# Optimization experiments

Measured on AMD Instinct MI355X. Metric: run time of the kernel, lower is better.

The kernel has to match this reference:

```python
import jax, jax.numpy as jnp
import numpy as np

NUM_VARS = 64
LAG = 16
H1 = 64
H2 = 1024
NUM_OUT = 1
BATCH = 16384


def setup_inputs() -> dict:
    key = jax.random.key(0)
    ks = jax.random.split(key, 8)

    def xavier(k, shape, fan_in, fan_out):
        std = float(np.sqrt(2.0 / (fan_in + fan_out)))
        return jax.random.normal(k, shape, dtype=jnp.float32) * std

    inputs = jax.random.normal(ks[0], (BATCH, NUM_VARS * LAG), dtype=jnp.float32)
    # Per-variable sub-network weights, batched over the variable axis.
    W1 = xavier(ks[1], (NUM_VARS, LAG, H1), LAG, H1)
    b1 = jnp.full((NUM_VARS, H1), 0.1, dtype=jnp.float32)
    W2 = xavier(ks[2], (NUM_VARS, H1, H1), H1, H1)
    b2 = jnp.full((NUM_VARS, H1), 0.1, dtype=jnp.float32)
    imp = (jnp.ones((NUM_VARS,), dtype=jnp.float32) / NUM_VARS
           + 1e-5 * jax.random.normal(ks[3], (NUM_VARS,), dtype=jnp.float32))
    W3 = xavier(ks[4], (NUM_VARS * H1, H2), NUM_VARS * H1, H2)
    b3 = jnp.full((H2,), 0.1, dtype=jnp.float32)
    W4 = xavier(ks[5], (H2, NUM_OUT), H2, NUM_OUT)
    b4 = jnp.full((NUM_OUT,), 0.1, dtype=jnp.float32)
    return {"inputs": inputs, "W1": W1, "b1": b1, "W2": W2, "b2": b2,
            "imp": imp, "W3": W3, "b3": b3, "W4": W4, "b4": b4}


def reference(inputs, W1, b1, W2, b2, imp, W3, b3, W4, b4):
    B = inputs.shape[0]
    # [B, V*lag] -> [B, V, lag]; slicing inputs[:, lag*i:lag*(i+1)] == x[:, i, :]
    x = inputs.reshape(B, NUM_VARS, LAG)
    # dp = 0.0 -> dropout is identity
    h = jax.nn.relu(jnp.einsum('bvl,vlh->bvh', x, W1) + b1[None])      # [B, V, H1]
    h = jax.nn.relu(jnp.einsum('bvh,vhk->bvk', h, W2) + b2[None])      # [B, V, H1]
    agg = (h * imp[None, :, None]).reshape(B, NUM_VARS * H1)            # weighted concat
    pred = jax.nn.relu(agg @ W3 + b3) @ W4 + b4                        # [B, NUM_OUT]
    return pred
```

## Files before the change

### kernel.cpp

```cpp
#include <hip/hip_runtime.h>
#include <hip/hip_bf16.h>
#include <stdint.h>

#define B_ROWS 16384
#define NVARS 64
#define LAG 16
#define H1 64
#define H2 1024
#define KDIM (NVARS * H1)

typedef __attribute__((ext_vector_type(8))) short short8;
typedef __attribute__((ext_vector_type(4))) short short4v;
typedef __attribute__((ext_vector_type(4))) float f32x4;

typedef __attribute__((address_space(3))) uint8_t lds_u8;
typedef const __attribute__((address_space(1))) uint8_t glob_u8;

__device__ __forceinline__ void gload_lds16(const void* g, void* l) {
    __builtin_amdgcn_global_load_lds((glob_u8*)g, (lds_u8*)l, 16, 0, 0);
}

__device__ __forceinline__ short f2bf_s(float x) {
    __hip_bfloat16 h = __float2bfloat16(x);
    return *(short*)&h;
}
__device__ __forceinline__ float bf_s2f(short s) {
    __hip_bfloat16 h = *(__hip_bfloat16*)&s;
    return __bfloat162float(h);
}

__global__ __launch_bounds__(256) void convert_w3t_kernel(
    const float* __restrict__ w3, __hip_bfloat16* __restrict__ w3t) {
    __shared__ float tile[64][65];
    const int bx = blockIdx.x;
    const int k0 = (bx >> 4) * 64;
    const int n0 = (bx & 15) * 64;
    const int t = threadIdx.x;
    const int c = t & 63, r0 = t >> 6;
#pragma unroll
    for (int i = 0; i < 16; i++) {
        int r = r0 + i * 4;
        tile[r][c] = w3[(size_t)(k0 + r) * H2 + n0 + c];
    }
    __syncthreads();
#pragma unroll
    for (int i = 0; i < 16; i++) {
        int nr = r0 + i * 4;
        w3t[(size_t)(n0 + nr) * KDIM + k0 + c] = __float2bfloat16(tile[c][nr]);
    }
}

__global__ __launch_bounds__(256) void prep_w12_kernel(
    const float* __restrict__ W1, const float* __restrict__ W2,
    short* __restrict__ w1bh, short* __restrict__ w1bl,
    short* __restrict__ w2bh, short* __restrict__ w2bl) {
    const int v = blockIdx.x, t = threadIdx.x;
    for (int idx = t; idx < 64 * 32; idx += 256) {
        int col = idx >> 5, k = idx & 31;
        float wv = W1[((size_t)v * LAG + (k & 15)) * H1 + col];
        short hi = f2bf_s(wv);
        w1bh[((size_t)v * 64 + col) * 40 + k] = hi;
        w1bl[((size_t)v * 64 + col) * 40 + k] = (k < 16) ? f2bf_s(wv - bf_s2f(hi)) : (short)0;
    }
    for (int idx = t; idx < 64 * 64; idx += 256) {
        int col = idx >> 6, k = idx & 63;
        float wv = W2[((size_t)v * H1 + k) * H1 + col];
        short hi = f2bf_s(wv);
        w2bh[((size_t)v * 64 + col) * 72 + k] = hi;
        w2bl[((size_t)v * 64 + col) * 72 + k] = f2bf_s(wv - bf_s2f(hi));
    }
}

__global__ __launch_bounds__(256) void out_init_kernel(
    const float* __restrict__ b4, float* __restrict__ out) {
    out[blockIdx.x * 256 + threadIdx.x] = b4[0];
}

__global__ __launch_bounds__(256) void subnets_mfma_kernel(
    const float* __restrict__ inputs, const float* __restrict__ b1g,
    const float* __restrict__ b2g, const float* __restrict__ impg,
    const short* __restrict__ w1bh_g, const short* __restrict__ w1bl_g,
    const short* __restrict__ w2bh_g, const short* __restrict__ w2bl_g,
    __hip_bfloat16* __restrict__ agg) {
    const int v = blockIdx.x >> 7;
    const int b0 = (blockIdx.x & 127) * 128;
    const int t = threadIdx.x;
    const int lane = t & 63, wv = t >> 6;
    const int l15 = lane & 15, g = lane >> 4;

    __shared__ __align__(16) char smem[53248];
    short* xsS   = (short*)smem;
    short* w1bhS = (short*)(smem + 10240);
    short* w1blS = (short*)(smem + 15360);
    short* Hs    = (short*)smem;
    short* w2bhS = (short*)(smem + 34816);
    short* w2blS = (short*)(smem + 44032);

    for (int c = t; c < 320; c += 256) {
        gload_lds16(w1bh_g + (size_t)v * 2560 + c * 8, (char*)w1bhS + c * 16);
        gload_lds16(w1bl_g + (size_t)v * 2560 + c * 8, (char*)w1blS + c * 16);
    }
    for (int c = t; c < 576; c += 256) {
        gload_lds16(w2bh_g + (size_t)v * 4608 + c * 8, (char*)w2bhS + c * 16);
        gload_lds16(w2bl_g + (size_t)v * 4608 + c * 8, (char*)w2blS + c * 16);
    }
#pragma unroll
    for (int i = 0; i < 2; i++) {
        int idx = t + i * 256;
        int row = idx >> 2, seg = idx & 3;
        float4 x4 = *(const float4*)(inputs + (size_t)(b0 + row) * (NVARS * LAG) + v * LAG + seg * 4);
        const float* xp = (const float*)&x4;
        short4v hv, lv;
#pragma unroll
        for (int j = 0; j < 4; j++) {
            short hi = f2bf_s(xp[j]);
            hv[j] = hi;
            lv[j] = f2bf_s(xp[j] - bf_s2f(hi));
        }
        *(short4v*)&xsS[row * 40 + seg * 4] = hv;
        *(short4v*)&xsS[row * 40 + 16 + seg * 4] = lv;
    }
    __syncthreads();

    short8 a1[2], b1hF[4], b1lF[4];
#pragma unroll
    for (int mt = 0; mt < 2; mt++)
        a1[mt] = *(const short8*)&xsS[(wv * 32 + mt * 16 + l15) * 40 + g * 8];
#pragma unroll
    for (int nt = 0; nt < 4; nt++) {
        b1hF[nt] = *(const short8*)&w1bhS[(nt * 16 + l15) * 40 + g * 8];
        b1lF[nt] = *(const short8*)&w1blS[(nt * 16 + l15) * 40 + g * 8];
    }
    f32x4 acc1[2][4];
#pragma unroll
    for (int mt = 0; mt < 2; mt++)
#pragma unroll
        for (int nt = 0; nt < 4; nt++) {
            acc1[mt][nt] = (f32x4){0.f, 0.f, 0.f, 0.f};
            acc1[mt][nt] = __builtin_amdgcn_mfma_f32_16x16x32_bf16(a1[mt], b1hF[nt], acc1[mt][nt], 0, 0, 0);
            acc1[mt][nt] = __builtin_amdgcn_mfma_f32_16x16x32_bf16(a1[mt], b1lF[nt], acc1[mt][nt], 0, 0, 0);
        }
    __syncthreads();

#pragma unroll
    for (int mt = 0; mt < 2; mt++)
#pragma unroll
        for (int nt = 0; nt < 4; nt++) {
            int col = nt * 16 + l15;
            float bias = b1g[v * H1 + col];
#pragma unroll
            for (int r = 0; r < 4; r++) {
                float h = fmaxf(acc1[mt][nt][r] + bias, 0.f);
                short hi = f2bf_s(h);
                short lo = f2bf_s(h - bf_s2f(hi));
                int row = wv * 32 + mt * 16 + g * 4 + r;
                Hs[row * 136 + col] = hi;
                Hs[row * 136 + 64 + col] = lo;
            }
        }
    __syncthreads();

    short8 a2[2][4], b2hF[4][2], b2lF[4][2];
#pragma unroll
    for (int mt = 0; mt < 2; mt++)
#pragma unroll
        for (int c = 0; c < 4; c++)
            a2[mt][c] = *(const short8*)&Hs[(wv * 32 + mt * 16 + l15) * 136 + c * 32 + g * 8];
#pragma unroll
    for (int nt = 0; nt < 4; nt++)
#pragma unroll
        for (int kc = 0; kc < 2; kc++) {
            b2hF[nt][kc] = *(const short8*)&w2bhS[(nt * 16 + l15) * 72 + kc * 32 + g * 8];
            b2lF[nt][kc] = *(const short8*)&w2blS[(nt * 16 + l15) * 72 + kc * 32 + g * 8];
        }
    f32x4 acc2[2][4];
#pragma unroll
    for (int mt = 0; mt < 2; mt++)
#pragma unroll
        for (int nt = 0; nt < 4; nt++) {
            f32x4 a = (f32x4){0.f, 0.f, 0.f, 0.f};
            a = __builtin_amdgcn_mfma_f32_16x16x32_bf16(a2[mt][0], b2hF[nt][0], a, 0, 0, 0);
            a = __builtin_amdgcn_mfma_f32_16x16x32_bf16(a2[mt][1], b2hF[nt][1], a, 0, 0, 0);
            a = __builtin_amdgcn_mfma_f32_16x16x32_bf16(a2[mt][2], b2hF[nt][0], a, 0, 0, 0);
            a = __builtin_amdgcn_mfma_f32_16x16x32_bf16(a2[mt][3], b2hF[nt][1], a, 0, 0, 0);
            a = __builtin_amdgcn_mfma_f32_16x16x32_bf16(a2[mt][0], b2lF[nt][0], a, 0, 0, 0);
            a = __builtin_amdgcn_mfma_f32_16x16x32_bf16(a2[mt][1], b2lF[nt][1], a, 0, 0, 0);
            acc2[mt][nt] = a;
        }

    const float impv = impg[v];
#pragma unroll
    for (int mt = 0; mt < 2; mt++)
#pragma unroll
        for (int nt = 0; nt < 4; nt++) {
            int col = nt * 16 + l15;
            float bias = b2g[v * H1 + col];
#pragma unroll
            for (int r = 0; r < 4; r++) {
                float o = fmaxf(acc2[mt][nt][r] + bias, 0.f) * impv;
                int row = b0 + wv * 32 + mt * 16 + g * 4 + r;
                agg[(size_t)row * KDIM + v * H1 + col] = __float2bfloat16(o);
            }
        }
}

#define NT 128

__global__ __launch_bounds__(512, 2) void gemm3_kernel(
    const __hip_bfloat16* __restrict__ agg,
    const __hip_bfloat16* __restrict__ w3t,
    const float* __restrict__ b3, const float* __restrict__ W4,
    float* __restrict__ out) {
    const int bid = ((blockIdx.x & 7) << 5) + (blockIdx.x >> 3);
    const int brow = (bid >> 2) * 256;
    const int bcol = (bid & 3) * 256;
    const int t = threadIdx.x;
    const int lane = t & 63;
    const int wid = t >> 6;
    const int wm = wid >> 2, wn = wid & 3;
    const int l15 = lane & 15, g = lane >> 4;

    __shared__ __align__(16) char smem[131072];

    const int c0 = t, c1 = t + 512;
    const int r0 = c0 >> 2, r1 = c1 >> 2;
    const int col0 = ((c0 & 3) * 8) ^ ((r0 & 8) ? 16 : 0);
    const int col1 = ((c1 & 3) * 8) ^ ((r1 & 8) ? 16 : 0);
    const __hip_bfloat16* aS0 = agg + (size_t)(brow + r0) * KDIM + col0;
    const __hip_bfloat16* aS1 = agg + (size_t)(brow + r1) * KDIM + col1;
    const __hip_bfloat16* bS0 = w3t + (size_t)(bcol + r0) * KDIM + col0;
    const __hip_bfloat16* bS1 = w3t + (size_t)(bcol + r1) * KDIM + col1;

#define STAGE_A(p, kt) do { \
        gload_lds16(aS0 + (kt) * 32, smem + (p) * 32768 + c0 * 16); \
        gload_lds16(aS1 + (kt) * 32, smem + (p) * 32768 + c1 * 16); } while (0)
#define STAGE_B(p, kt) do { \
        gload_lds16(bS0 + (kt) * 32, smem + (p) * 32768 + 16384 + c0 * 16); \
        gload_lds16(bS1 + (kt) * 32, smem + (p) * 32768 + 16384 + c1 * 16); } while (0)

    const int coff = (g * 16) ^ ((l15 & 8) ? 32 : 0);
    const int aBase = (wm * 128 + l15) * 64 + coff;
    const int bBase = 16384 + (wn * 64 + l15) * 64 + coff;

#define LDA(i, p) fa[i] = *(const short8*)(smem + (p) * 32768 + aBase + (i) * 1024)
#define LDB(i, p) fb[i] = *(const short8*)(smem + (p) * 32768 + bBase + (i) * 1024)

    short8 fa[8], fb[4];
    f32x4 acc[8][4];
#pragma unroll
    for (int m = 0; m < 8; m++)
#pragma unroll
        for (int n = 0; n < 4; n++) acc[m][n] = (f32x4){0.f, 0.f, 0.f, 0.f};

    STAGE_A(0, 0); STAGE_B(0, 0);
    STAGE_A(1, 1); STAGE_B(1, 1);
    STAGE_A(2, 2); STAGE_B(2, 2);
    asm volatile("s_waitcnt vmcnt(8)" ::: "memory");
    __builtin_amdgcn_s_barrier();

#define PH_A(p, DOSTAGE, kt3) do { \
        LDA(0, p); LDA(1, p); LDA(2, p); LDA(3, p); \
        LDB(0, p); LDB(1, p); LDB(2, p); LDB(3, p); \
        if (DOSTAGE) STAGE_A((kt3) & 3, kt3); \
        __builtin_amdgcn_s_barrier(); \
        asm volatile("s_waitcnt lgkmcnt(0)" ::: "memory"); \
        __builtin_amdgcn_sched_barrier(0); \
        __builtin_amdgcn_s_setprio(1); \
        _Pragma("unroll") \
        for (int mm = 0; mm < 4; mm++) \
            _Pragma("unroll") \
            for (int nn = 0; nn < 4; nn++) \
                acc[mm][nn] = __builtin_amdgcn_mfma_f32_16x16x32_bf16( \
                    fa[mm], fb[nn], acc[mm][nn], 0, 0, 0); \
        __builtin_amdgcn_s_setprio(0); \
        __builtin_amdgcn_s_barrier(); } while (0)

#define PH_B(p, DOSTAGE, kt3, VMSTR) do { \
        LDA(4, p); LDA(5, p); LDA(6, p); LDA(7, p); \
        if (DOSTAGE) STAGE_B((kt3) & 3, kt3); \
        asm volatile(VMSTR ::: "memory"); \
        __builtin_amdgcn_s_barrier(); \
        asm volatile("s_waitcnt lgkmcnt(0)" ::: "memory"); \
        __builtin_amdgcn_sched_barrier(0); \
        __builtin_amdgcn_s_setprio(1); \
        _Pragma("unroll") \
        for (int mm = 0; mm < 4; mm++) \
            _Pragma("unroll") \
            for (int nn = 0; nn < 4; nn++) \
                acc[4 + mm][nn] = __builtin_amdgcn_mfma_f32_16x16x32_bf16( \
                    fa[4 + mm], fb[nn], acc[4 + mm][nn], 0, 0, 0); \
        __builtin_amdgcn_s_setprio(0); \
        __builtin_amdgcn_s_barrier(); } while (0)

#pragma unroll 4
    for (int tt = 0; tt < NT - 4; ++tt) {
        const int p = tt & 3;
        PH_A(p, 1, tt + 3);
        PH_B(p, 1, tt + 3, "s_waitcnt vmcnt(8)");
    }
    PH_A(0, 1, 127); PH_B(0, 1, 127, "s_waitcnt vmcnt(8)");
    PH_A(1, 0, 0);   PH_B(1, 0, 0, "s_waitcnt vmcnt(4)");
    PH_A(2, 0, 0);   PH_B(2, 0, 0, "s_waitcnt vmcnt(0)");
    PH_A(3, 0, 0);   PH_B(3, 0, 0, "s_waitcnt vmcnt(0)");

    float bias[4], w4v[4];
#pragma unroll
    for (int n = 0; n < 4; n++) {
        int col = bcol + wn * 64 + n * 16 + l15;
        bias[n] = b3[col];
        w4v[n] = W4[col];
    }
#pragma unroll
    for (int m = 0; m < 8; m++) {
        float pr0 = 0.f, pr1 = 0.f, pr2 = 0.f, pr3 = 0.f;
#pragma unroll
        for (int n = 0; n < 4; n++) {
            pr0 += fmaxf(acc[m][n][0] + bias[n], 0.f) * w4v[n];
            pr1 += fmaxf(acc[m][n][1] + bias[n], 0.f) * w4v[n];
            pr2 += fmaxf(acc[m][n][2] + bias[n], 0.f) * w4v[n];
            pr3 += fmaxf(acc[m][n][3] + bias[n], 0.f) * w4v[n];
        }
#pragma unroll
        for (int mask = 1; mask < 16; mask <<= 1) {
            pr0 += __shfl_xor(pr0, mask, 64);
            pr1 += __shfl_xor(pr1, mask, 64);
            pr2 += __shfl_xor(pr2, mask, 64);
            pr3 += __shfl_xor(pr3, mask, 64);
        }
        if (l15 == 0) {
            int row = brow + wm * 128 + m * 16 + g * 4;
            atomicAdd(&out[row + 0], pr0);
            atomicAdd(&out[row + 1], pr1);
            atomicAdd(&out[row + 2], pr2);
            atomicAdd(&out[row + 3], pr3);
        }
    }
}

extern "C" void kernel_launch(void* const* d_in, const int* in_sizes, int n_in,
                              void* d_out, int out_size, void* d_ws, size_t ws_size,
                              hipStream_t stream) {
    const float* inputs = (const float*)d_in[0];
    const float* W1 = (const float*)d_in[1];
    const float* b1 = (const float*)d_in[2];
    const float* W2 = (const float*)d_in[3];
    const float* b2 = (const float*)d_in[4];
    const float* imp = (const float*)d_in[5];
    const float* W3 = (const float*)d_in[6];
    const float* b3 = (const float*)d_in[7];
    const float* W4 = (const float*)d_in[8];
    const float* b4 = (const float*)d_in[9];
    float* out = (float*)d_out;

    char* ws = (char*)d_ws;
    const size_t agg_bytes  = (size_t)B_ROWS * KDIM * 2;
    const size_t w3t_bytes  = (size_t)H2 * KDIM * 2;
    const size_t w1b_bytes  = (size_t)NVARS * 64 * 40 * 2;
    const size_t w2b_bytes  = (size_t)NVARS * 64 * 72 * 2;

    __hip_bfloat16* agg = (__hip_bfloat16*)ws;
    __hip_bfloat16* w3t = (__hip_bfloat16*)(ws + agg_bytes);
    short* w1bh = (short*)(ws + agg_bytes + w3t_bytes);
    short* w1bl = (short*)(ws + agg_bytes + w3t_bytes + w1b_bytes);
    short* w2bh = (short*)(ws + agg_bytes + w3t_bytes + 2 * w1b_bytes);
    short* w2bl = (short*)(ws + agg_bytes + w3t_bytes + 2 * w1b_bytes + w2b_bytes);

    hipLaunchKernelGGL(convert_w3t_kernel, dim3(1024), dim3(256), 0, stream, W3, w3t);
    hipLaunchKernelGGL(prep_w12_kernel, dim3(NVARS), dim3(256), 0, stream,
                       W1, W2, w1bh, w1bl, w2bh, w2bl);
    hipLaunchKernelGGL(out_init_kernel, dim3(B_ROWS / 256), dim3(256), 0, stream, b4, out);
    hipLaunchKernelGGL(subnets_mfma_kernel, dim3(NVARS * (B_ROWS / 128)), dim3(256), 0, stream,
                       inputs, b1, b2, imp, w1bh, w1bl, w2bh, w2bl, agg);
    hipLaunchKernelGGL(gemm3_kernel, dim3((B_ROWS / 256) * (H2 / 256)), dim3(512), 0, stream,
                       agg, w3t, b3, W4, out);
}
```

Before: 181.4 us.

## Fuse preprocessing kernels into one launch and cut GEMM pipeline barriers

Merges the W3 transpose/convert, the output bias init and the subnet kernel into a single launch, dispatched by block-index ranges. W1/W2 are now split into hi/lo bf16 directly into LDS inside each subnet block, which removes the separate prep kernel and its workspace round trip at the cost of redundant per-block conversion. In the GEMM main loop, the per-phase barriers and explicit lgkmcnt waits are replaced by a single vmcnt wait plus barrier at the end of each iteration. This relies on the 4-deep buffer ring to keep LDS staging writes away from buffers still being read.

```diff
diff --git a/kernel.cpp b/kernel.cpp
--- a/kernel.cpp
+++ b/kernel.cpp
@@ -29,66 +29,46 @@
     return __bfloat162float(h);
 }
 
-__global__ __launch_bounds__(256) void convert_w3t_kernel(
-    const float* __restrict__ w3, __hip_bfloat16* __restrict__ w3t) {
-    __shared__ float tile[64][65];
-    const int bx = blockIdx.x;
-    const int k0 = (bx >> 4) * 64;
-    const int n0 = (bx & 15) * 64;
+__global__ __launch_bounds__(256) void fused_pre_kernel(
+    const float* __restrict__ inputs, const float* __restrict__ W1,
+    const float* __restrict__ b1g, const float* __restrict__ W2,
+    const float* __restrict__ b2g, const float* __restrict__ impg,
+    const float* __restrict__ w3, const float* __restrict__ b4,
+    __hip_bfloat16* __restrict__ w3t, __hip_bfloat16* __restrict__ agg,
+    float* __restrict__ out) {
+    __shared__ __align__(16) char smem[53248];
+    const int bid = blockIdx.x;
     const int t = threadIdx.x;
-    const int c = t & 63, r0 = t >> 6;
-#pragma unroll
-    for (int i = 0; i < 16; i++) {
-        int r = r0 + i * 4;
-        tile[r][c] = w3[(size_t)(k0 + r) * H2 + n0 + c];
-    }
-    __syncthreads();
-#pragma unroll
-    for (int i = 0; i < 16; i++) {
-        int nr = r0 + i * 4;
-        w3t[(size_t)(n0 + nr) * KDIM + k0 + c] = __float2bfloat16(tile[c][nr]);
-    }
-}
-
-__global__ __launch_bounds__(256) void prep_w12_kernel(
-    const float* __restrict__ W1, const float* __restrict__ W2,
-    short* __restrict__ w1bh, short* __restrict__ w1bl,
-    short* __restrict__ w2bh, short* __restrict__ w2bl) {
-    const int v = blockIdx.x, t = threadIdx.x;
-    for (int idx = t; idx < 64 * 32; idx += 256) {
-        int col = idx >> 5, k = idx & 31;
-        float wv = W1[((size_t)v * LAG + (k & 15)) * H1 + col];
-        short hi = f2bf_s(wv);
-        w1bh[((size_t)v * 64 + col) * 40 + k] = hi;
-        w1bl[((size_t)v * 64 + col) * 40 + k] = (k < 16) ? f2bf_s(wv - bf_s2f(hi)) : (short)0;
-    }
-    for (int idx = t; idx < 64 * 64; idx += 256) {
-        int col = idx >> 6, k = idx & 63;
-        float wv = W2[((size_t)v * H1 + k) * H1 + col];
-        short hi = f2bf_s(wv);
-        w2bh[((size_t)v * 64 + col) * 72 + k] = hi;
-        w2bl[((size_t)v * 64 + col) * 72 + k] = f2bf_s(wv - bf_s2f(hi));
-    }
-}
-
-__global__ __launch_bounds__(256) void out_init_kernel(
-    const float* __restrict__ b4, float* __restrict__ out) {
-    out[blockIdx.x * 256 + threadIdx.x] = b4[0];
-}
-
-__global__ __launch_bounds__(256) void subnets_mfma_kernel(
-    const float* __restrict__ inputs, const float* __restrict__ b1g,
-    const float* __restrict__ b2g, const float* __restrict__ impg,
-    const short* __restrict__ w1bh_g, const short* __restrict__ w1bl_g,
-    const short* __restrict__ w2bh_g, const short* __restrict__ w2bl_g,
-    __hip_bfloat16* __restrict__ agg) {
-    const int v = blockIdx.x >> 7;
-    const int b0 = (blockIdx.x & 127) * 128;
-    const int t = threadIdx.x;
+
+    if (bid < 1024) {
+        float (*tile)[65] = (float (*)[65])smem;
+        const int k0 = (bid >> 4) * 64;
+        const int n0 = (bid & 15) * 64;
+        const int c = t & 63, r0 = t >> 6;
+#pragma unroll
+        for (int i = 0; i < 16; i++) {
+            int r = r0 + i * 4;
+            tile[r][c] = w3[(size_t)(k0 + r) * H2 + n0 + c];
+        }
+        __syncthreads();
+#pragma unroll
+        for (int i = 0; i < 16; i++) {
+            int nr = r0 + i * 4;
+            w3t[(size_t)(n0 + nr) * KDIM + k0 + c] = __float2bfloat16(tile[c][nr]);
+        }
+        return;
+    }
+    if (bid < 1088) {
+        out[(bid - 1024) * 256 + t] = b4[0];
+        return;
+    }
+
+    const int sbid = bid - 1088;
+    const int v = sbid >> 7;
+    const int b0 = (sbid & 127) * 128;
     const int lane = t & 63, wv = t >> 6;
     const int l15 = lane & 15, g = lane >> 4;
 
-    __shared__ __align__(16) char smem[53248];
     short* xsS   = (short*)smem;
     short* w1bhS = (short*)(smem + 10240);
     short* w1blS = (short*)(smem + 15360);
@@ -96,13 +76,21 @@
     short* w2bhS = (short*)(smem + 34816);
     short* w2blS = (short*)(smem + 44032);
 
-    for (int c = t; c < 320; c += 256) {
-        gload_lds16(w1bh_g + (size_t)v * 2560 + c * 8, (char*)w1bhS + c * 16);
-        gload_lds16(w1bl_g + (size_t)v * 2560 + c * 8, (char*)w1blS + c * 16);
-    }
-    for (int c = t; c < 576; c += 256) {
-        gload_lds16(w2bh_g + (size_t)v * 4608 + c * 8, (char*)w2bhS + c * 16);
-        gload_lds16(w2bl_g + (size_t)v * 4608 + c * 8, (char*)w2blS + c * 16);
+    for (int idx = t; idx < LAG * H1; idx += 256) {
+        int l = idx >> 6, col = idx & 63;
+        float w = W1[(size_t)v * (LAG * H1) + idx];
+        short hi = f2bf_s(w), lo = f2bf_s(w - bf_s2f(hi));
+        w1bhS[col * 40 + l] = hi;
+        w1bhS[col * 40 + 16 + l] = hi;
+        w1blS[col * 40 + l] = lo;
+        w1blS[col * 40 + 16 + l] = 0;
+    }
+    for (int idx = t; idx < H1 * H1; idx += 256) {
+        int k = idx >> 6, col = idx & 63;
+        float w = W2[(size_t)v * (H1 * H1) + idx];
+        short hi = f2bf_s(w), lo = f2bf_s(w - bf_s2f(hi));
+        w2bhS[col * 72 + k] = hi;
+        w2blS[col * 72 + k] = lo;
     }
 #pragma unroll
     for (int i = 0; i < 2; i++) {
@@ -257,14 +245,12 @@
     STAGE_A(2, 2); STAGE_B(2, 2);
     asm volatile("s_waitcnt vmcnt(8)" ::: "memory");
     __builtin_amdgcn_s_barrier();
+    __builtin_amdgcn_sched_barrier(0);
 
 #define PH_A(p, DOSTAGE, kt3) do { \
         LDA(0, p); LDA(1, p); LDA(2, p); LDA(3, p); \
         LDB(0, p); LDB(1, p); LDB(2, p); LDB(3, p); \
         if (DOSTAGE) STAGE_A((kt3) & 3, kt3); \
-        __builtin_amdgcn_s_barrier(); \
-        asm volatile("s_waitcnt lgkmcnt(0)" ::: "memory"); \
-        __builtin_amdgcn_sched_barrier(0); \
         __builtin_amdgcn_s_setprio(1); \
         _Pragma("unroll") \
         for (int mm = 0; mm < 4; mm++) \
@@ -272,16 +258,11 @@
             for (int nn = 0; nn < 4; nn++) \
                 acc[mm][nn] = __builtin_amdgcn_mfma_f32_16x16x32_bf16( \
                     fa[mm], fb[nn], acc[mm][nn], 0, 0, 0); \
-        __builtin_amdgcn_s_setprio(0); \
-        __builtin_amdgcn_s_barrier(); } while (0)
+        __builtin_amdgcn_s_setprio(0); } while (0)
 
 #define PH_B(p, DOSTAGE, kt3, VMSTR) do { \
         LDA(4, p); LDA(5, p); LDA(6, p); LDA(7, p); \
         if (DOSTAGE) STAGE_B((kt3) & 3, kt3); \
-        asm volatile(VMSTR ::: "memory"); \
-        __builtin_amdgcn_s_barrier(); \
-        asm volatile("s_waitcnt lgkmcnt(0)" ::: "memory"); \
-        __builtin_amdgcn_sched_barrier(0); \
         __builtin_amdgcn_s_setprio(1); \
         _Pragma("unroll") \
         for (int mm = 0; mm < 4; mm++) \
@@ -290,7 +271,9 @@
                 acc[4 + mm][nn] = __builtin_amdgcn_mfma_f32_16x16x32_bf16( \
                     fa[4 + mm], fb[nn], acc[4 + mm][nn], 0, 0, 0); \
         __builtin_amdgcn_s_setprio(0); \
-        __builtin_amdgcn_s_barrier(); } while (0)
+        asm volatile(VMSTR ::: "memory"); \
+        __builtin_amdgcn_s_barrier(); \
+        __builtin_amdgcn_sched_barrier(0); } while (0)
 
 #pragma unroll 4
     for (int tt = 0; tt < NT - 4; ++tt) {
@@ -353,24 +336,12 @@
     float* out = (float*)d_out;
 
     char* ws = (char*)d_ws;
-    const size_t agg_bytes  = (size_t)B_ROWS * KDIM * 2;
-    const size_t w3t_bytes  = (size_t)H2 * KDIM * 2;
-    const size_t w1b_bytes  = (size_t)NVARS * 64 * 40 * 2;
-    const size_t w2b_bytes  = (size_t)NVARS * 64 * 72 * 2;
-
+    const size_t agg_bytes = (size_t)B_ROWS * KDIM * 2;
     __hip_bfloat16* agg = (__hip_bfloat16*)ws;
     __hip_bfloat16* w3t = (__hip_bfloat16*)(ws + agg_bytes);
-    short* w1bh = (short*)(ws + agg_bytes + w3t_bytes);
-    short* w1bl = (short*)(ws + agg_bytes + w3t_bytes + w1b_bytes);
-    short* w2bh = (short*)(ws + agg_bytes + w3t_bytes + 2 * w1b_bytes);
-    short* w2bl = (short*)(ws + agg_bytes + w3t_bytes + 2 * w1b_bytes + w2b_bytes);
-
-    hipLaunchKernelGGL(convert_w3t_kernel, dim3(1024), dim3(256), 0, stream, W3, w3t);
-    hipLaunchKernelGGL(prep_w12_kernel, dim3(NVARS), dim3(256), 0, stream,
-                       W1, W2, w1bh, w1bl, w2bh, w2bl);
-    hipLaunchKernelGGL(out_init_kernel, dim3(B_ROWS / 256), dim3(256), 0, stream, b4, out);
-    hipLaunchKernelGGL(subnets_mfma_kernel, dim3(NVARS * (B_ROWS / 128)), dim3(256), 0, stream,
-                       inputs, b1, b2, imp, w1bh, w1bl, w2bh, w2bl, agg);
+
+    hipLaunchKernelGGL(fused_pre_kernel, dim3(1088 + NVARS * (B_ROWS / 128)), dim3(256), 0, stream,
+                       inputs, W1, b1, W2, b2, imp, W3, b4, w3t, agg, out);
     hipLaunchKernelGGL(gemm3_kernel, dim3((B_ROWS / 256) * (H2 / 256)), dim3(512), 0, stream,
                        agg, w3t, b3, W4, out);
 }
```

Result: no change. 184.4 us (+1.6%).

## Cut gemm3 pipeline barriers to one per k-step and merge prep kernels

Applied to the files above, without the earlier changes.

The main W3 GEMM loop previously used four workgroup barriers per k-step, plus explicit lgkmcnt waits before each MFMA block. It now has a single barrier and vmcnt wait at the end of each k-step, relying on the 4-deep LDS ring to keep staging writes from racing with reads. Separately, the W3 transpose/convert, W1/W2 split-bf16 prep and output bias init kernels are fused into one launch that dispatches on block index, saving two launches. The looser sync lets waves drift apart more. Correctness depends on the ring-buffer reuse distance being large enough.

```diff
diff --git a/kernel.cpp b/kernel.cpp
--- a/kernel.cpp
+++ b/kernel.cpp
@@ -29,32 +29,39 @@
     return __bfloat162float(h);
 }
 
-__global__ __launch_bounds__(256) void convert_w3t_kernel(
-    const float* __restrict__ w3, __hip_bfloat16* __restrict__ w3t) {
-    __shared__ float tile[64][65];
-    const int bx = blockIdx.x;
-    const int k0 = (bx >> 4) * 64;
-    const int n0 = (bx & 15) * 64;
-    const int t = threadIdx.x;
-    const int c = t & 63, r0 = t >> 6;
-#pragma unroll
-    for (int i = 0; i < 16; i++) {
-        int r = r0 + i * 4;
-        tile[r][c] = w3[(size_t)(k0 + r) * H2 + n0 + c];
-    }
-    __syncthreads();
-#pragma unroll
-    for (int i = 0; i < 16; i++) {
-        int nr = r0 + i * 4;
-        w3t[(size_t)(n0 + nr) * KDIM + k0 + c] = __float2bfloat16(tile[c][nr]);
-    }
-}
-
-__global__ __launch_bounds__(256) void prep_w12_kernel(
+__global__ __launch_bounds__(256) void misc_pre_kernel(
+    const float* __restrict__ w3, const float* __restrict__ b4,
     const float* __restrict__ W1, const float* __restrict__ W2,
+    __hip_bfloat16* __restrict__ w3t, float* __restrict__ out,
     short* __restrict__ w1bh, short* __restrict__ w1bl,
     short* __restrict__ w2bh, short* __restrict__ w2bl) {
-    const int v = blockIdx.x, t = threadIdx.x;
+    __shared__ float tile[64][65];
+    const int bid = blockIdx.x;
+    const int t = threadIdx.x;
+
+    if (bid < 1024) {
+        const int k0 = (bid >> 4) * 64;
+        const int n0 = (bid & 15) * 64;
+        const int c = t & 63, r0 = t >> 6;
+#pragma unroll
+        for (int i = 0; i < 16; i++) {
+            int r = r0 + i * 4;
+            tile[r][c] = w3[(size_t)(k0 + r) * H2 + n0 + c];
+        }
+        __syncthreads();
+#pragma unroll
+        for (int i = 0; i < 16; i++) {
+            int nr = r0 + i * 4;
+            w3t[(size_t)(n0 + nr) * KDIM + k0 + c] = __float2bfloat16(tile[c][nr]);
+        }
+        return;
+    }
+    if (bid < 1088) {
+        out[(bid - 1024) * 256 + t] = b4[0];
+        return;
+    }
+
+    const int v = bid - 1088;
     for (int idx = t; idx < 64 * 32; idx += 256) {
         int col = idx >> 5, k = idx & 31;
         float wv = W1[((size_t)v * LAG + (k & 15)) * H1 + col];
@@ -69,11 +76,6 @@
         w2bh[((size_t)v * 64 + col) * 72 + k] = hi;
         w2bl[((size_t)v * 64 + col) * 72 + k] = f2bf_s(wv - bf_s2f(hi));
     }
-}
-
-__global__ __launch_bounds__(256) void out_init_kernel(
-    const float* __restrict__ b4, float* __restrict__ out) {
-    out[blockIdx.x * 256 + threadIdx.x] = b4[0];
 }
 
 __global__ __launch_bounds__(256) void subnets_mfma_kernel(
@@ -257,14 +259,12 @@
     STAGE_A(2, 2); STAGE_B(2, 2);
     asm volatile("s_waitcnt vmcnt(8)" ::: "memory");
     __builtin_amdgcn_s_barrier();
+    __builtin_amdgcn_sched_barrier(0);
 
 #define PH_A(p, DOSTAGE, kt3) do { \
         LDA(0, p); LDA(1, p); LDA(2, p); LDA(3, p); \
         LDB(0, p); LDB(1, p); LDB(2, p); LDB(3, p); \
         if (DOSTAGE) STAGE_A((kt3) & 3, kt3); \
-        __builtin_amdgcn_s_barrier(); \
-        asm volatile("s_waitcnt lgkmcnt(0)" ::: "memory"); \
-        __builtin_amdgcn_sched_barrier(0); \
         __builtin_amdgcn_s_setprio(1); \
         _Pragma("unroll") \
         for (int mm = 0; mm < 4; mm++) \
@@ -272,16 +272,11 @@
             for (int nn = 0; nn < 4; nn++) \
                 acc[mm][nn] = __builtin_amdgcn_mfma_f32_16x16x32_bf16( \
                     fa[mm], fb[nn], acc[mm][nn], 0, 0, 0); \
-        __builtin_amdgcn_s_setprio(0); \
-        __builtin_amdgcn_s_barrier(); } while (0)
+        __builtin_amdgcn_s_setprio(0); } while (0)
 
 #define PH_B(p, DOSTAGE, kt3, VMSTR) do { \
         LDA(4, p); LDA(5, p); LDA(6, p); LDA(7, p); \
         if (DOSTAGE) STAGE_B((kt3) & 3, kt3); \
-        asm volatile(VMSTR ::: "memory"); \
-        __builtin_amdgcn_s_barrier(); \
-        asm volatile("s_waitcnt lgkmcnt(0)" ::: "memory"); \
-        __builtin_amdgcn_sched_barrier(0); \
         __builtin_amdgcn_s_setprio(1); \
         _Pragma("unroll") \
         for (int mm = 0; mm < 4; mm++) \
@@ -290,7 +285,9 @@
                 acc[4 + mm][nn] = __builtin_amdgcn_mfma_f32_16x16x32_bf16( \
                     fa[4 + mm], fb[nn], acc[4 + mm][nn], 0, 0, 0); \
         __builtin_amdgcn_s_setprio(0); \
-        __builtin_amdgcn_s_barrier(); } while (0)
+        asm volatile(VMSTR ::: "memory"); \
+        __builtin_amdgcn_s_barrier(); \
+        __builtin_amdgcn_sched_barrier(0); } while (0)
 
 #pragma unroll 4
     for (int tt = 0; tt < NT - 4; ++tt) {
@@ -353,10 +350,10 @@
     float* out = (float*)d_out;
 
     char* ws = (char*)d_ws;
-    const size_t agg_bytes  = (size_t)B_ROWS * KDIM * 2;
-    const size_t w3t_bytes  = (size_t)H2 * KDIM * 2;
-    const size_t w1b_bytes  = (size_t)NVARS * 64 * 40 * 2;
-    const size_t w2b_bytes  = (size_t)NVARS * 64 * 72 * 2;
+    const size_t agg_bytes = (size_t)B_ROWS * KDIM * 2;
+    const size_t w3t_bytes = (size_t)H2 * KDIM * 2;
+    const size_t w1b_bytes = (size_t)NVARS * 64 * 40 * 2;
+    const size_t w2b_bytes = (size_t)NVARS * 64 * 72 * 2;
 
     __hip_bfloat16* agg = (__hip_bfloat16*)ws;
     __hip_bfloat16* w3t = (__hip_bfloat16*)(ws + agg_bytes);
@@ -365,10 +362,8 @@
     short* w2bh = (short*)(ws + agg_bytes + w3t_bytes + 2 * w1b_bytes);
     short* w2bl = (short*)(ws + agg_bytes + w3t_bytes + 2 * w1b_bytes + w2b_bytes);
 
-    hipLaunchKernelGGL(convert_w3t_kernel, dim3(1024), dim3(256), 0, stream, W3, w3t);
-    hipLaunchKernelGGL(prep_w12_kernel, dim3(NVARS), dim3(256), 0, stream,
-                       W1, W2, w1bh, w1bl, w2bh, w2bl);
-    hipLaunchKernelGGL(out_init_kernel, dim3(B_ROWS / 256), dim3(256), 0, stream, b4, out);
+    hipLaunchKernelGGL(misc_pre_kernel, dim3(1152), dim3(256), 0, stream,
+                       W3, b4, W1, W2, w3t, out, w1bh, w1bl, w2bh, w2bl);
     hipLaunchKernelGGL(subnets_mfma_kernel, dim3(NVARS * (B_ROWS / 128)), dim3(256), 0, stream,
                        inputs, b1, b2, imp, w1bh, w1bl, w2bh, w2bl, agg);
     hipLaunchKernelGGL(gemm3_kernel, dim3((B_ROWS / 256) * (H2 / 256)), dim3(512), 0, stream,
```

New measurement: 179.2 us. No clear change (-1.2%).
